# Optimization experiments

Hardware: AMD Instinct MI355X
Metric: run time of the kernel (lower is better)

## Reference

```python
import jax, jax.numpy as jnp
import numpy as np

N, C, D = 131072, 512, 3


def setup_inputs() -> dict:
    key = jax.random.key(0)
    kx, kmu = jax.random.split(key)
    X = jax.random.normal(kx, (N, D), dtype=jnp.float32)
    mu = jax.random.normal(kmu, (C, D), dtype=jnp.float32)
    w = jnp.zeros((C,), dtype=jnp.float32)
    # sigma as in __init__: r = sqrt(sum of per-dim unbiased variances of mu0)
    r = jnp.sqrt(jnp.var(mu, axis=0, ddof=1).sum())
    sigma = (0.1 * (r / C ** (1.0 / D))).astype(jnp.float32)
    return {"X": X, "mu": mu, "w": w, "sigma": sigma}


def reference(X, mu, w, sigma):
    # One EM step of a uniform-covariance GMM (EM_step_pytorch).
    n, d = X.shape
    # pairwise squared distances [N, C]
    D2_nc = ((X[:, None, :] - mu[None, :, :]) ** 2).sum(-1)
    # log-responsibilities (E-step), softmax over components
    lgamma_nc = jax.nn.log_softmax(w[None, :] - D2_nc / (2.0 * sigma ** 2), axis=1)
    gamma_nc = jnp.exp(lgamma_nc)
    # M-step: centroids (softmax over points, per component)
    mu_new = jax.nn.softmax(lgamma_nc, axis=0).T @ X  # [C, D]
    # M-step: component scores
    h_c = jax.nn.logsumexp(lgamma_nc, axis=0)  # [C]
    w_new = h_c - h_c.mean()
    # M-step: uniform std
    sigma_new = jnp.sqrt((gamma_nc * D2_nc).sum() / (d * n))
    # EM values: expected targets and free energy
    Y = gamma_nc @ mu_new  # [N, D]
    logpi_c = w_new - jax.nn.logsumexp(w_new)
    Cfe = (gamma_nc * (
        ((mu_new ** 2).sum(-1)[None, :] - (Y ** 2).sum(-1)[:, None]) / (2.0 * sigma_new ** 2)
        + d * jnp.log(sigma_new)
        - logpi_c[None, :]
        + lgamma_nc
    )).sum()
    return Y, Cfe
```

## Files before the change

kernel.cpp:

```cpp
#include <hip/hip_runtime.h>
#include <cfloat>
#include <cmath>

#define NPTS 131072
#define NC   512
#define NREP 4
#define L2E  1.4426950408889634f
#define LN2  0.6931471805599453f
#define CUT  34.0f
#define ECAP 2048
#define PK   15

#define PM4_OFF  0
#define PQ4_OFF  2048
#define ST4_OFF  4096
#define MISC_OFF 12288
#define PL_OFF   16384

__device__ __forceinline__ float waveSum(float v) {
#pragma unroll
  for (int off = 32; off > 0; off >>= 1) v += __shfl_down(v, off, 64);
  return v;
}
__device__ __forceinline__ float waveMax(float v) {
#pragma unroll
  for (int off = 32; off > 0; off >>= 1) v = fmaxf(v, __shfl_down(v, off, 64));
  return v;
}
__device__ __forceinline__ unsigned lanePrefix(unsigned long long m) {
  return __builtin_amdgcn_mbcnt_hi(
      (unsigned)(m >> 32), __builtin_amdgcn_mbcnt_lo((unsigned)m, 0u));
}

__global__ __launch_bounds__(512) void k_prep(
    const float* __restrict__ mu, const float* __restrict__ w,
    const float* __restrict__ sigma, float4* __restrict__ pm,
    float* __restrict__ ST, float* __restrict__ misc) {
  const int t = threadIdx.x;
  const float sg = sigma[0];
  const float k2 = L2E / (2.0f * sg * sg);
  const float m0 = mu[3 * t], m1 = mu[3 * t + 1], m2 = mu[3 * t + 2];
  pm[t] = make_float4(2.0f * k2 * m0, 2.0f * k2 * m1, 2.0f * k2 * m2,
                      w[t] * L2E - (m0 * m0 + m1 * m1 + m2 * m2) * k2);
#pragma unroll
  for (int r = 0; r < NREP * 4; ++r) ST[r * 512 + t] = 0.f;
  if (t < 8) misc[t] = 0.f;
}

__global__ __launch_bounds__(512, 4) void k_estep(
    const float* __restrict__ X, const float4* __restrict__ pm,
    float* __restrict__ ST, float* __restrict__ misc,
    float* __restrict__ out, unsigned short* __restrict__ plist) {
  __shared__ float4 s_pt[128];
  __shared__ float  s_m[4][128];
  __shared__ float2 s_sq[4][128];
  __shared__ float  s_M[128];
  __shared__ unsigned int s_cnt;
  __shared__ unsigned int s_pcnt[128];
  __shared__ unsigned int s_ec[ECAP];
  __shared__ float        s_el[ECAP];

  const int t = threadIdx.x;
  const int p = t & 127;
  const int ch = __builtin_amdgcn_readfirstlane(t >> 7);
  const int n = blockIdx.x * 128 + p;
  const float x0 = X[3 * n], x1 = X[3 * n + 1], x2 = X[3 * n + 2];

  if (t == 0) s_cnt = 0u;
  if (t < 128) {
    s_pcnt[t] = 0u;
    s_pt[t] = make_float4(x0, x1, x2, 0.f);
  }

  const float4* __restrict__ pmc = pm + ch * 128;
  float ma = -FLT_MAX, mb = -FLT_MAX, mc2 = -FLT_MAX, md = -FLT_MAX;
#pragma unroll 4
  for (int i = 0; i < 128; i += 4) {
    float4 a = pmc[i], b = pmc[i + 1], c = pmc[i + 2], d = pmc[i + 3];
    ma  = fmaxf(ma,  fmaf(a.x, x0, fmaf(a.y, x1, fmaf(a.z, x2, a.w))));
    mb  = fmaxf(mb,  fmaf(b.x, x0, fmaf(b.y, x1, fmaf(b.z, x2, b.w))));
    mc2 = fmaxf(mc2, fmaf(c.x, x0, fmaf(c.y, x1, fmaf(c.z, x2, c.w))));
    md  = fmaxf(md,  fmaf(d.x, x0, fmaf(d.y, x1, fmaf(d.z, x2, d.w))));
  }
  s_m[ch][p] = fmaxf(fmaxf(ma, mb), fmaxf(mc2, md));
  __syncthreads();

  if (t < 128) {
    s_M[t] = fmaxf(fmaxf(s_m[0][t], s_m[1][t]), fmaxf(s_m[2][t], s_m[3][t]));
  }
  __syncthreads();

  const float M = s_M[p];
  const float thr = M - CUT;
  const int cbase = ch * 128;

  float sE = 0.f, qE = 0.f;
#pragma unroll 2
  for (int i = 0; i < 128; ++i) {
    float4 a = pmc[i];
    const float l = fmaf(a.x, x0, fmaf(a.y, x1, fmaf(a.z, x2, a.w)));
    const bool hit = (l >= thr);
    const unsigned long long mask = __ballot(hit);
    if (mask) {
      const float d = l - M;
      const float e = exp2f(d);
      sE += e;
      qE = fmaf(e, d, qE);
      unsigned base;
      if ((t & 63) == 0) base = atomicAdd(&s_cnt, (unsigned)__popcll(mask));
      base = __builtin_amdgcn_readfirstlane(base);
      if (hit) {
        const unsigned idx = base + lanePrefix(mask);
        if (idx < (unsigned)ECAP) {
          s_ec[idx] = ((unsigned)p << 16) | (unsigned)(cbase + i);
          s_el[idx] = l;
        }
      }
    }
  }
  s_sq[ch][p] = make_float2(sE, qE);
  __syncthreads();

  if (t < 128) {
    float2 q0 = s_sq[0][t], q1 = s_sq[1][t], q2 = s_sq[2][t], q3 = s_sq[3][t];
    const float ss = (q0.x + q1.x) + (q2.x + q3.x);
    const float qq = (q0.y + q1.y) + (q2.y + q3.y);
    const float lg = __log2f(ss);
    const float z = s_M[t] + lg;
    s_pt[t].w = z;
    out[3 * n] = z;
    const float La = LN2 * (__fdividef(qq, ss) - lg);
    const float xx = x0 * x0 + x1 * x1 + x2 * x2;
    const float rl = waveSum(La);
    const float rx = waveSum(xx);
    if ((t & 63) == 0) { atomicAdd(&misc[3], rl); atomicAdd(&misc[0], rx); }
  }
  __syncthreads();

  const unsigned total = min(s_cnt, (unsigned)ECAP);
  float* __restrict__ stbase = ST + ((blockIdx.x & (NREP - 1)) * 512) * 4;
  const int bn = blockIdx.x * 128;
  for (unsigned idx = t; idx < total; idx += 512) {
    const unsigned ec = s_ec[idx];
    const unsigned pp = ec >> 16;
    const unsigned c = ec & 0xFFFFu;
    const float4 pt = s_pt[pp];
    const float g = exp2f(s_el[idx] - pt.w);
    float* st = stbase + c * 4;
    atomicAdd(st + 0, g * pt.x);
    atomicAdd(st + 1, g * pt.y);
    atomicAdd(st + 2, g * pt.z);
    atomicAdd(st + 3, g);
    if (plist) {
      const unsigned slot = atomicAdd(&s_pcnt[pp], 1u);
      if (slot < (unsigned)PK)
        plist[(size_t)(bn + pp) * 16u + 1u + slot] = (unsigned short)c;
    }
  }
  __syncthreads();
  if (plist && t < 128) {
    const unsigned pc = s_pcnt[t];
    plist[(size_t)(bn + t) * 16u] =
        (pc > (unsigned)PK) ? (unsigned short)0xFFFFu : (unsigned short)pc;
  }
}

__global__ __launch_bounds__(512) void k_mstep(
    const float* __restrict__ mu, const float4* __restrict__ ST4,
    float4* __restrict__ pq, float* __restrict__ misc,
    float* __restrict__ out) {
  __shared__ float s_red[8];
  __shared__ float s_red2[8];
  __shared__ float s_bc[4];
  const int t = threadIdx.x;

  float Tx = 0.f, Ty = 0.f, Tz = 0.f, S = 0.f;
#pragma unroll
  for (int r = 0; r < NREP; ++r) {
    float4 v = ST4[r * 512 + t];
    Tx += v.x; Ty += v.y; Tz += v.z; S += v.w;
  }
  const float Sc = fmaxf(S, 1e-30f);
  const float h = __logf(Sc);
  const float m0 = Tx / Sc, m1 = Ty / Sc, m2 = Tz / Sc;

  const float o0 = mu[3 * t], o1 = mu[3 * t + 1], o2 = mu[3 * t + 2];
  const float gdp = S * (o0 * o0 + o1 * o1 + o2 * o2)
                    - 2.0f * (o0 * Tx + o1 * Ty + o2 * Tz);

  float hm = waveMax(h);
  if ((t & 63) == 0) s_red[t >> 6] = hm;
  __syncthreads();
  if (t == 0) {
    float v = s_red[0];
    for (int i = 1; i < 8; ++i) v = fmaxf(v, s_red[i]);
    s_bc[0] = v;
  }
  __syncthreads();
  const float hM = s_bc[0];

  float es = waveSum(__expf(h - hM));
  float gs = waveSum(gdp);
  if ((t & 63) == 0) { s_red[t >> 6] = es; s_red2[t >> 6] = gs; }
  __syncthreads();
  if (t == 0) {
    float esum = 0.f, gsum = 0.f;
    for (int i = 0; i < 8; ++i) { esum += s_red[i]; gsum += s_red2[i]; }
    s_bc[1] = hM + __logf(esum);
    const float gd = fmaxf(misc[0] + gsum, 1e-20f);
    const float sn2 = gd * (1.0f / (3.0f * (float)NPTS));
    s_bc[2] = 1.0f / (2.0f * sn2);
    s_bc[3] = 1.5f * __logf(sn2);
  }
  __syncthreads();

  const float inv2s2n = s_bc[2];
  const float logpi = h - s_bc[1];
  const float A = (m0 * m0 + m1 * m1 + m2 * m2) * inv2s2n - logpi;
  pq[t] = make_float4(m0, m1, m2, A);

  float ca = waveSum(S * A);
  if ((t & 63) == 0) s_red[t >> 6] = ca;
  __syncthreads();
  if (t == 0) {
    float v = 0.f;
    for (int i = 0; i < 8; ++i) v += s_red[i];
    out[NPTS * 3] = v + misc[3] + (float)NPTS * s_bc[3];
    misc[1] = inv2s2n;
  }
}

__global__ __launch_bounds__(512, 4) void k_final_list(
    const float* __restrict__ X, const float4* __restrict__ pm,
    const float4* __restrict__ pq, const float* __restrict__ misc,
    float* __restrict__ out, const unsigned short* __restrict__ plist) {
  __shared__ float4 s_pm[NC];
  __shared__ float4 s_pq[NC];
  __shared__ float  s_red[8];

  const int t = threadIdx.x;
  const int n = blockIdx.x * 512 + t;

  s_pm[t] = pm[t];
  s_pq[t] = pq[t];

  const float x0 = X[3 * n], x1 = X[3 * n + 1], x2 = X[3 * n + 2];
  const float z = out[3 * n];
  const float inv2s2n = misc[1];

  const uint4* __restrict__ lp =
      reinterpret_cast<const uint4*>(plist) + ((size_t)n << 1);
  const uint4 wA = lp[0];
  const uint4 wB = lp[1];
  unsigned int words[8] = {wA.x, wA.y, wA.z, wA.w, wB.x, wB.y, wB.z, wB.w};
  const unsigned int cnt = words[0] & 0xFFFFu;
  __syncthreads();

  float y0 = 0.f, y1 = 0.f, y2 = 0.f;
  if (cnt == 0xFFFFu) {
    const float thr = z - CUT;
    for (int c = 0; c < NC; ++c) {
      float4 pp = s_pm[c];
      const float l = fmaf(pp.x, x0, fmaf(pp.y, x1, fmaf(pp.z, x2, pp.w)));
      if (l >= thr) {
        const float g = exp2f(l - z);
        float4 qq = s_pq[c];
        y0 = fmaf(g, qq.x, y0);
        y1 = fmaf(g, qq.y, y1);
        y2 = fmaf(g, qq.z, y2);
      }
    }
  } else {
    const int ic = (int)cnt;
#pragma unroll
    for (int j = 0; j < PK; ++j) {
      if (!__any(j < ic)) break;
      if (j < ic) {
        const unsigned int word = words[(j + 1) >> 1];
        const unsigned int c =
            ((j + 1) & 1) ? (word >> 16) : (word & 0xFFFFu);
        float4 pp = s_pm[c];
        const float l = fmaf(pp.x, x0, fmaf(pp.y, x1, fmaf(pp.z, x2, pp.w)));
        const float g = exp2f(l - z);
        float4 qq = s_pq[c];
        y0 = fmaf(g, qq.x, y0);
        y1 = fmaf(g, qq.y, y1);
        y2 = fmaf(g, qq.z, y2);
      }
    }
  }

  const float cfe = -(y0 * y0 + y1 * y1 + y2 * y2) * inv2s2n;
  out[3 * n] = y0;
  out[3 * n + 1] = y1;
  out[3 * n + 2] = y2;

  float r = waveSum(cfe);
  if ((t & 63) == 0) s_red[t >> 6] = r;
  __syncthreads();
  if (t == 0) {
    float v = 0.f;
#pragma unroll
    for (int i = 0; i < 8; ++i) v += s_red[i];
    atomicAdd(&out[NPTS * 3], v);
  }
}

__global__ __launch_bounds__(512, 8) void k_final_dense(
    const float* __restrict__ X, const float4* __restrict__ pm,
    const float4* __restrict__ pq, const float* __restrict__ misc,
    float* __restrict__ out) {
  __shared__ float4 s_y[4][128];
  __shared__ float  s_red[8];

  const int t = threadIdx.x;
  const int p = t & 127;
  const int ch = __builtin_amdgcn_readfirstlane(t >> 7);
  const int n = blockIdx.x * 128 + p;
  const float x0 = X[3 * n], x1 = X[3 * n + 1], x2 = X[3 * n + 2];
  const float z = out[3 * n];
  const float inv2s2n = misc[1];

  const float4* __restrict__ pmc = pm + ch * 128;
  const float4* __restrict__ pqc = pq + ch * 128;
  float y0 = 0.f, y1 = 0.f, y2 = 0.f;
#pragma unroll 4
  for (int i = 0; i < 128; ++i) {
    float4 pp = pmc[i];
    float4 qq = pqc[i];
    const float l = fmaf(pp.x, x0, fmaf(pp.y, x1, fmaf(pp.z, x2, pp.w))) - z;
    const float g = exp2f(l);
    y0 = fmaf(g, qq.x, y0);
    y1 = fmaf(g, qq.y, y1);
    y2 = fmaf(g, qq.z, y2);
  }
  s_y[ch][p] = make_float4(y0, y1, y2, 0.f);
  __syncthreads();

  float cfe = 0.f;
  if (t < 128) {
    float4 a0 = s_y[0][t], a1 = s_y[1][t], a2 = s_y[2][t], a3 = s_y[3][t];
    const float Y0 = (a0.x + a1.x) + (a2.x + a3.x);
    const float Y1 = (a0.y + a1.y) + (a2.y + a3.y);
    const float Y2 = (a0.z + a1.z) + (a2.z + a3.z);
    cfe = -(Y0 * Y0 + Y1 * Y1 + Y2 * Y2) * inv2s2n;
    out[3 * n] = Y0;
    out[3 * n + 1] = Y1;
    out[3 * n + 2] = Y2;
  }
  float r = waveSum(cfe);
  if ((t & 63) == 0) s_red[t >> 6] = r;
  __syncthreads();
  if (t == 0) {
    float v = 0.f;
#pragma unroll
    for (int i = 0; i < 8; ++i) v += s_red[i];
    atomicAdd(&out[NPTS * 3], v);
  }
}

extern "C" void kernel_launch(void* const* d_in, const int* in_sizes, int n_in,
                              void* d_out, int out_size, void* d_ws, size_t ws_size,
                              hipStream_t stream) {
  const float* X = (const float*)d_in[0];
  const float* mu = (const float*)d_in[1];
  const float* w = (const float*)d_in[2];
  const float* sigma = (const float*)d_in[3];
  float* out = (float*)d_out;
  float* ws = (float*)d_ws;

  float4* pm = (float4*)(ws + PM4_OFF);
  float4* pq = (float4*)(ws + PQ4_OFF);
  float* ST = ws + ST4_OFF;
  float* misc = ws + MISC_OFF;

  const size_t need = (size_t)PL_OFF * 4 + (size_t)NPTS * 32;
  unsigned short* plist =
      (ws_size >= need) ? (unsigned short*)(ws + PL_OFF) : (unsigned short*)0;

  k_prep<<<1, 512, 0, stream>>>(mu, w, sigma, pm, ST, misc);
  k_estep<<<NPTS / 128, 512, 0, stream>>>(X, pm, ST, misc, out, plist);
  k_mstep<<<1, 512, 0, stream>>>(mu, (const float4*)ST, pq, misc, out);
  if (plist)
    k_final_list<<<NPTS / 512, 512, 0, stream>>>(X, pm, pq, misc, out, plist);
  else
    k_final_dense<<<NPTS / 128, 512, 0, stream>>>(X, pm, pq, misc, out);
}
```

Before: 158.8 us.

## Replace per-iteration ballot/atomic compaction with bitmask sweep and per-wave slots

The E-step sweep no longer does a ballot, branch and shared atomic per component. It now computes exp2 for every component and records hits in 32-bit masks. Hits are compacted afterwards by iterating set bits with per-wave private slots of 256 entries, recomputing the logit for each hit, and the scatter loop reads per-wave counts. This removes divergence and shared-atomic contention from the hot loop. In exchange it evaluates exp2 unconditionally, adds a second pass over hits, and caps overflow per wave rather than per block.

```diff
diff --git a/kernel.cpp b/kernel.cpp
--- a/kernel.cpp
+++ b/kernel.cpp
@@ -8,7 +8,8 @@
 #define L2E  1.4426950408889634f
 #define LN2  0.6931471805599453f
 #define CUT  34.0f
-#define ECAP 2048
+#define WSL  256
+#define ECAP (8 * WSL)
 #define PK   15
 
 #define PM4_OFF  0
@@ -30,6 +31,23 @@
 __device__ __forceinline__ unsigned lanePrefix(unsigned long long m) {
   return __builtin_amdgcn_mbcnt_hi(
       (unsigned)(m >> 32), __builtin_amdgcn_mbcnt_lo((unsigned)m, 0u));
+}
+
+__device__ __forceinline__ unsigned sweep32(
+    const float4* __restrict__ pmc, float x0, float x1, float x2,
+    float M, float thr, float& sE, float& qE) {
+  unsigned m = 0u;
+#pragma unroll 8
+  for (int i = 0; i < 32; ++i) {
+    float4 a = pmc[i];
+    const float l = fmaf(a.x, x0, fmaf(a.y, x1, fmaf(a.z, x2, a.w)));
+    const float d = l - M;
+    const float e = exp2f(d);
+    sE += e;
+    qE = fmaf(e, d, qE);
+    m = (m >> 1) | ((l >= thr) ? 0x80000000u : 0u);
+  }
+  return m;
 }
 
 __global__ __launch_bounds__(512) void k_prep(
@@ -55,18 +73,19 @@
   __shared__ float  s_m[4][128];
   __shared__ float2 s_sq[4][128];
   __shared__ float  s_M[128];
-  __shared__ unsigned int s_cnt;
-  __shared__ unsigned int s_pcnt[128];
-  __shared__ unsigned int s_ec[ECAP];
-  __shared__ float        s_el[ECAP];
+  __shared__ unsigned s_wcnt[8];
+  __shared__ unsigned s_pcnt[128];
+  __shared__ unsigned s_ec[ECAP];
+  __shared__ float    s_el[ECAP];
 
   const int t = threadIdx.x;
   const int p = t & 127;
   const int ch = __builtin_amdgcn_readfirstlane(t >> 7);
+  const int wv = t >> 6;
+  const unsigned wbase = (unsigned)wv * WSL;
   const int n = blockIdx.x * 128 + p;
   const float x0 = X[3 * n], x1 = X[3 * n + 1], x2 = X[3 * n + 2];
 
-  if (t == 0) s_cnt = 0u;
   if (t < 128) {
     s_pcnt[t] = 0u;
     s_pt[t] = make_float4(x0, x1, x2, 0.f);
@@ -92,33 +111,44 @@
 
   const float M = s_M[p];
   const float thr = M - CUT;
-  const int cbase = ch * 128;
+  const unsigned cbase = (unsigned)(ch * 128);
 
   float sE = 0.f, qE = 0.f;
-#pragma unroll 2
-  for (int i = 0; i < 128; ++i) {
-    float4 a = pmc[i];
-    const float l = fmaf(a.x, x0, fmaf(a.y, x1, fmaf(a.z, x2, a.w)));
-    const bool hit = (l >= thr);
-    const unsigned long long mask = __ballot(hit);
-    if (mask) {
-      const float d = l - M;
-      const float e = exp2f(d);
-      sE += e;
-      qE = fmaf(e, d, qE);
-      unsigned base;
-      if ((t & 63) == 0) base = atomicAdd(&s_cnt, (unsigned)__popcll(mask));
-      base = __builtin_amdgcn_readfirstlane(base);
-      if (hit) {
-        const unsigned idx = base + lanePrefix(mask);
-        if (idx < (unsigned)ECAP) {
-          s_ec[idx] = ((unsigned)p << 16) | (unsigned)(cbase + i);
-          s_el[idx] = l;
-        }
-      }
-    }
-  }
+  const unsigned mk0 = sweep32(pmc +  0, x0, x1, x2, M, thr, sE, qE);
+  const unsigned mk1 = sweep32(pmc + 32, x0, x1, x2, M, thr, sE, qE);
+  const unsigned mk2 = sweep32(pmc + 64, x0, x1, x2, M, thr, sE, qE);
+  const unsigned mk3 = sweep32(pmc + 96, x0, x1, x2, M, thr, sE, qE);
   s_sq[ch][p] = make_float2(sE, qE);
+
+  unsigned long long mA = (unsigned long long)mk0 |
+                          ((unsigned long long)mk1 << 32);
+  unsigned long long mB = (unsigned long long)mk2 |
+                          ((unsigned long long)mk3 << 32);
+  unsigned wcnt = 0u;
+
+#define PROC(mreg, cb)                                                       \
+  while (true) {                                                             \
+    const unsigned long long wm = __ballot((mreg) != 0ull);                  \
+    if (!wm) break;                                                          \
+    const bool act = ((mreg) != 0ull);                                       \
+    unsigned ii = 0u;                                                        \
+    if (act) { ii = (unsigned)__builtin_ctzll(mreg); (mreg) &= (mreg) - 1; } \
+    const unsigned pos = wcnt + lanePrefix(wm);                              \
+    wcnt += (unsigned)__popcll(wm);                                          \
+    if (act && pos < (unsigned)WSL) {                                        \
+      const unsigned c = (cb) + ii;                                          \
+      const float4 a = pm[c];                                                \
+      const float l = fmaf(a.x, x0, fmaf(a.y, x1, fmaf(a.z, x2, a.w)));      \
+      s_ec[wbase + pos] = ((unsigned)p << 16) | c;                           \
+      s_el[wbase + pos] = l;                                                 \
+    }                                                                        \
+  }
+
+  PROC(mA, cbase)
+  PROC(mB, cbase + 64u)
+#undef PROC
+
+  if ((t & 63) == 0) s_wcnt[wv] = wcnt;
   __syncthreads();
 
   if (t < 128) {
@@ -137,24 +167,28 @@
   }
   __syncthreads();
 
-  const unsigned total = min(s_cnt, (unsigned)ECAP);
   float* __restrict__ stbase = ST + ((blockIdx.x & (NREP - 1)) * 512) * 4;
   const int bn = blockIdx.x * 128;
-  for (unsigned idx = t; idx < total; idx += 512) {
-    const unsigned ec = s_ec[idx];
-    const unsigned pp = ec >> 16;
-    const unsigned c = ec & 0xFFFFu;
-    const float4 pt = s_pt[pp];
-    const float g = exp2f(s_el[idx] - pt.w);
-    float* st = stbase + c * 4;
-    atomicAdd(st + 0, g * pt.x);
-    atomicAdd(st + 1, g * pt.y);
-    atomicAdd(st + 2, g * pt.z);
-    atomicAdd(st + 3, g);
-    if (plist) {
-      const unsigned slot = atomicAdd(&s_pcnt[pp], 1u);
-      if (slot < (unsigned)PK)
-        plist[(size_t)(bn + pp) * 16u + 1u + slot] = (unsigned short)c;
+#pragma unroll
+  for (unsigned idx = (unsigned)t; idx < (unsigned)ECAP; idx += 512u) {
+    const unsigned w2 = idx >> 8;
+    const unsigned j = idx & (WSL - 1u);
+    if (j < s_wcnt[w2]) {
+      const unsigned ec = s_ec[idx];
+      const unsigned pp = ec >> 16;
+      const unsigned c = ec & 0xFFFFu;
+      const float4 pt = s_pt[pp];
+      const float g = exp2f(s_el[idx] - pt.w);
+      float* st = stbase + c * 4;
+      atomicAdd(st + 0, g * pt.x);
+      atomicAdd(st + 1, g * pt.y);
+      atomicAdd(st + 2, g * pt.z);
+      atomicAdd(st + 3, g);
+      if (plist) {
+        const unsigned slot = atomicAdd(&s_pcnt[pp], 1u);
+        if (slot < (unsigned)PK)
+          plist[(size_t)(bn + pp) * 16u + 1u + slot] = (unsigned short)c;
+      }
     }
   }
   __syncthreads();
```

Measured after the change: 166.1 us. +4.6%, slower.
